# Kernel optimization log

Measured on AMD Instinct MI355X. Metric: run time of the kernel, lower is better.

Reference implementation:

```python
import jax, jax.numpy as jnp
import numpy as np

B, T, N, C, D = 8, 12, 1024, 64, 10

def setup_inputs() -> dict:
    key = jax.random.key(0)
    ks = jax.random.split(key, 7)
    x = jax.random.normal(ks[0], (B, T, N, C), dtype=jnp.float32)
    e1 = jax.random.normal(ks[1], (N, D), dtype=jnp.float32)
    e2 = jax.random.normal(ks[2], (N, D), dtype=jnp.float32)
    # buffer: sym-normalized adjacency after the __init__-time softmax
    A_sym = jax.random.uniform(ks[3], (N, N), dtype=jnp.float32)
    weights_pool = jax.random.normal(ks[4], (N, C, C), dtype=jnp.float32) * 0.02
    bias_pool = jax.random.normal(ks[5], (N, C), dtype=jnp.float32) * 0.02
    alpha = jnp.array([0.9], dtype=jnp.float32)
    beta = jnp.array([0.9], dtype=jnp.float32)
    gamma = jnp.array([0.1], dtype=jnp.float32)
    return {"x": x, "node_embeddings1": e1, "node_embeddings2": e2,
            "A_sym": A_sym, "weights_pool": weights_pool, "bias_pool": bias_pool,
            "alpha": alpha, "beta": beta, "gamma": gamma}


def reference(x, node_embeddings1, node_embeddings2, A_sym, weights_pool,
              bias_pool, alpha, beta, gamma):
    n = node_embeddings1.shape[0]
    # dynamic supports: relu(tanh(E1 E2^T - E2 E1^T)) + I
    s = jnp.tanh(node_embeddings1 @ node_embeddings2.T
                 - node_embeddings2 @ node_embeddings1.T)
    supports = jnp.eye(n, dtype=x.dtype) + jax.nn.relu(s)          # (N,N)

    # static branch: row-softmax of the precomputed sym-norm adjacency
    A = jax.nn.softmax(A_sym, axis=-1)                              # (N,N)
    x_static = jax.nn.relu(jnp.einsum('nm,btmc->btnc', A, x))       # (B,T,N,C)

    # spatial attention branch (note: softmax over the TIME axis, as in source)
    score = jnp.einsum('btnc,btmc->btnm', x, x)                     # (B,T,N,N)
    score = jax.nn.softmax(score, axis=1)
    x_sa = jax.nn.relu(jnp.einsum('btnm,btmc->btnc', score, x))     # (B,T,N,C)

    # adaptive graph conv: per-node weights/bias from supports
    weights = jnp.einsum('nd,dio->nio', supports, weights_pool)     # (N,C,C)
    bias = supports @ bias_pool                                     # (N,C)
    x_g = jnp.einsum('nm,btmc->btnc', supports, x)                  # (B,T,N,C)
    x_gconv = jax.nn.relu(jnp.einsum('btni,nio->btno', x_g, weights) + bias)

    return alpha * x_gconv + beta * x_sa + gamma * x_static
```

## Files before the change

### kernel.cpp

```cpp
#include <hip/hip_runtime.h>
#include <math.h>

#define Bdim 8
#define Tdim 12
#define BT   96
#define Ndim 1024
#define Cdim 64
#define Ddim 10
#define Jdim 6144
#define IOdim 4096

typedef __attribute__((ext_vector_type(4))) float f32x4;
typedef __attribute__((ext_vector_type(8))) short bf16x8;
typedef __attribute__((ext_vector_type(4))) _Float16 f16x4;

__device__ inline short f2bf(float f) {
    union { float f; unsigned u; } v; v.f = f;
    return (short)((v.u + 0x8000u) >> 16);
}
__device__ inline float bf2f(short s) {
    union { float f; unsigned u; } v; v.u = ((unsigned)(unsigned short)s) << 16;
    return v.f;
}
__device__ inline void load_lds16(const void* g, void* l) {
    __builtin_amdgcn_global_load_lds(
        (const __attribute__((address_space(1))) unsigned int*)g,
        (__attribute__((address_space(3))) unsigned int*)l, 16, 0, 0);
}
__device__ inline float fexp(float x) { return __expf(x); }
__device__ inline float frcp(float x) { return __builtin_amdgcn_rcpf(x); }
__device__ inline float flog(float x) { return __logf(x); }

__global__ __launch_bounds__(256) void k_supports(
    const float* __restrict__ e1, const float* __restrict__ e2,
    short* __restrict__ Sbf)
{
    int idx = blockIdx.x * 256 + threadIdx.x;
    int i = idx >> 10, j = idx & 1023;
    float s = 0.f;
#pragma unroll
    for (int d = 0; d < Ddim; ++d)
        s += e1[i * Ddim + d] * e2[j * Ddim + d]
           - e2[i * Ddim + d] * e1[j * Ddim + d];
    float t = 1.f - 2.f * frcp(fexp(2.f * s) + 1.f);
    float v = fmaxf(t, 0.f);
    if (i == j) v += 1.f;
    Sbf[idx] = f2bf(v);
}

__global__ __launch_bounds__(256) void k_softmax_rows(
    const float* __restrict__ In, short* __restrict__ Out)
{
    int row = blockIdx.x;
    const float* r = In + (size_t)row * Ndim;
    short* o = Out + (size_t)row * Ndim;
    __shared__ float red[256];
    int tid = threadIdx.x;
    float vals[4];
    float lmax = -INFINITY;
#pragma unroll
    for (int i = 0; i < 4; ++i) { vals[i] = r[tid + 256 * i]; lmax = fmaxf(lmax, vals[i]); }
    red[tid] = lmax; __syncthreads();
    for (int s = 128; s > 0; s >>= 1) {
        if (tid < s) red[tid] = fmaxf(red[tid], red[tid + s]);
        __syncthreads();
    }
    float m = red[0]; __syncthreads();
    float lsum = 0.f;
#pragma unroll
    for (int i = 0; i < 4; ++i) { vals[i] = fexp(vals[i] - m); lsum += vals[i]; }
    red[tid] = lsum; __syncthreads();
    for (int s = 128; s > 0; s >>= 1) {
        if (tid < s) red[tid] += red[tid + s];
        __syncthreads();
    }
    float inv = frcp(red[0]);
#pragma unroll
    for (int i = 0; i < 4; ++i) o[tid + 256 * i] = f2bf(vals[i] * inv);
}

__global__ __launch_bounds__(256) void k_cvt_x(
    const float* __restrict__ x, short* __restrict__ xbf, short* __restrict__ xT)
{
    __shared__ float Lt[64][65];
    int bt = blockIdx.y, n0 = blockIdx.x * 64;
    const float* src = x + (size_t)bt * 65536 + (size_t)n0 * 64;
    int tid = threadIdx.x;
#pragma unroll
    for (int p = 0; p < 4; ++p) {
        int idx = p * 256 + tid;
        int r = idx >> 4, c4 = idx & 15;
        float4 v = *(const float4*)&src[r * 64 + c4 * 4];
        short4 s4 = make_short4(f2bf(v.x), f2bf(v.y), f2bf(v.z), f2bf(v.w));
        *(short4*)&xbf[(size_t)bt * 65536 + (size_t)(n0 + r) * 64 + c4 * 4] = s4;
        Lt[r][c4 * 4 + 0] = v.x; Lt[r][c4 * 4 + 1] = v.y;
        Lt[r][c4 * 4 + 2] = v.z; Lt[r][c4 * 4 + 3] = v.w;
    }
    __syncthreads();
#pragma unroll
    for (int p = 0; p < 4; ++p) {
        int idx = p * 256 + tid;
        int c = idx >> 4, k4 = idx & 15;
        short4 s4 = make_short4(f2bf(Lt[k4 * 4 + 0][c]), f2bf(Lt[k4 * 4 + 1][c]),
                                f2bf(Lt[k4 * 4 + 2][c]), f2bf(Lt[k4 * 4 + 3][c]));
        *(short4*)&xT[(size_t)bt * 65536 + (size_t)c * 1024 + n0 + k4 * 4] = s4;
    }
}

__global__ __launch_bounds__(256) void k_cvt_wp(
    const float* __restrict__ wp, short* __restrict__ wpT)
{
    __shared__ float Lt[64][65];
    int k0 = blockIdx.y * 64, j0 = blockIdx.x * 64;
    int tid = threadIdx.x;
#pragma unroll
    for (int p = 0; p < 4; ++p) {
        int idx = p * 256 + tid;
        int r = idx >> 4, c4 = idx & 15;
        float4 v = *(const float4*)&wp[(size_t)(k0 + r) * IOdim + j0 + c4 * 4];
        Lt[r][c4 * 4 + 0] = v.x; Lt[r][c4 * 4 + 1] = v.y;
        Lt[r][c4 * 4 + 2] = v.z; Lt[r][c4 * 4 + 3] = v.w;
    }
    __syncthreads();
#pragma unroll
    for (int p = 0; p < 4; ++p) {
        int idx = p * 256 + tid;
        int c = idx >> 4, k4 = idx & 15;
        short4 s4 = make_short4(f2bf(Lt[k4 * 4 + 0][c]), f2bf(Lt[k4 * 4 + 1][c]),
                                f2bf(Lt[k4 * 4 + 2][c]), f2bf(Lt[k4 * 4 + 3][c]));
        *(short4*)&wpT[(size_t)(j0 + c) * 1024 + k0 + k4 * 4] = s4;
    }
}

__global__ __launch_bounds__(256) void k_cvt_bp(
    const float* __restrict__ bp, short* __restrict__ bpT)
{
    __shared__ float Lt[64][65];
    int k0 = blockIdx.x * 64;
    int tid = threadIdx.x;
#pragma unroll
    for (int p = 0; p < 4; ++p) {
        int idx = p * 256 + tid;
        int r = idx >> 4, c4 = idx & 15;
        float4 v = *(const float4*)&bp[(size_t)(k0 + r) * 64 + c4 * 4];
        Lt[r][c4 * 4 + 0] = v.x; Lt[r][c4 * 4 + 1] = v.y;
        Lt[r][c4 * 4 + 2] = v.z; Lt[r][c4 * 4 + 3] = v.w;
    }
    __syncthreads();
#pragma unroll
    for (int p = 0; p < 4; ++p) {
        int idx = p * 256 + tid;
        int c = idx >> 4, k4 = idx & 15;
        short4 s4 = make_short4(f2bf(Lt[k4 * 4 + 0][c]), f2bf(Lt[k4 * 4 + 1][c]),
                                f2bf(Lt[k4 * 4 + 2][c]), f2bf(Lt[k4 * 4 + 3][c]));
        *(short4*)&bpT[(size_t)c * 1024 + k0 + k4 * 4] = s4;
    }
}

template<int MODE>
__global__ __launch_bounds__(256) void k_gemm_bt(
    const short* __restrict__ A, const short* __restrict__ Bm,
    float* __restrict__ Cf, short* __restrict__ Cb,
    const float* __restrict__ gamma_p)
{
    __shared__ short At[128 * 64];
    __shared__ short Bt[128 * 64];
    const int tid = threadIdx.x;
    const int w = tid >> 6, l = tid & 63;
    const int l15 = l & 15, q = l >> 4;
    const int n0 = blockIdx.x * 128, j0 = blockIdx.y * 128;
    const int wr = (w & 1) * 64, wc = (w >> 1) * 64;
    const int lrow = l >> 3, lc8 = l & 7;

    f32x4 acc[4][4];
#pragma unroll
    for (int i = 0; i < 4; ++i)
#pragma unroll
        for (int j = 0; j < 4; ++j) acc[i][j] = (f32x4)0.f;

    for (int k0 = 0; k0 < 1024; k0 += 64) {
        __syncthreads();
#pragma unroll
        for (int p = 0; p < 4; ++p) {
            int r = p * 32 + w * 8 + lrow;
            int sc = lc8 ^ (r & 7);
            load_lds16(A + (size_t)(n0 + r) * 1024 + k0 + sc * 8,
                       &At[(p * 32 + w * 8) * 64]);
            load_lds16(Bm + (size_t)(j0 + r) * 1024 + k0 + sc * 8,
                       &Bt[(p * 32 + w * 8) * 64]);
        }
        __syncthreads();
#pragma unroll
        for (int ks = 0; ks < 2; ++ks) {
            bf16x8 af[4], bf[4];
#pragma unroll
            for (int rt = 0; rt < 4; ++rt) {
                int row = wr + rt * 16 + l15;
                int pos = (ks * 4 + q) ^ (row & 7);
                af[rt] = *(const bf16x8*)&At[row * 64 + pos * 8];
            }
#pragma unroll
            for (int ct = 0; ct < 4; ++ct) {
                int row = wc + ct * 16 + l15;
                int pos = (ks * 4 + q) ^ (row & 7);
                bf[ct] = *(const bf16x8*)&Bt[row * 64 + pos * 8];
            }
#pragma unroll
            for (int rt = 0; rt < 4; ++rt)
#pragma unroll
                for (int ct = 0; ct < 4; ++ct)
                    acc[rt][ct] = __builtin_amdgcn_mfma_f32_16x16x32_bf16(
                        af[rt], bf[ct], acc[rt][ct], 0, 0, 0);
        }
    }

    float gmm = (MODE == 0) ? gamma_p[0] : 0.f;
#pragma unroll
    for (int rt = 0; rt < 4; ++rt) {
        int nr = n0 + wr + rt * 16 + q * 4;
#pragma unroll
        for (int ct = 0; ct < 4; ++ct) {
            int j = j0 + wc + ct * 16 + l15;
#pragma unroll
            for (int r = 0; r < 4; ++r) {
                float v = acc[rt][ct][r];
                int n = nr + r;
                if (MODE == 1) {
                    Cb[(size_t)n * IOdim + j] = f2bf(v);
                } else if (n < 1024) {
                    int bt = j >> 6, c = j & 63;
                    Cf[(size_t)bt * 65536 + (size_t)n * 64 + c] = gmm * fmaxf(v, 0.f);
                } else {
                    Cb[(size_t)(n - 1024) * Jdim + j] = f2bf(v);
                }
            }
        }
    }
}

__global__ __launch_bounds__(256, 4) void k_sa_z(
    const short* __restrict__ xbf, short* __restrict__ Lh)
{
    __shared__ short Xn[64 * 64];
    __shared__ short Xm[64 * 64];

    int id = blockIdx.x;
    int b = id & 7;
    int r = id >> 3;
    int tn = r & 15, tm = r >> 4;
    int tid = threadIdx.x;
    int w = tid >> 6, l = tid & 63;
    int l15 = l & 15, q = l >> 4;
    int lrow = l >> 3, lc8 = l & 7;
    int n0 = tn * 64, m0 = tm * 64;
    int wn = (w & 1) * 32, wm = (w >> 1) * 32;

    const short* Xb = xbf + (size_t)b * Tdim * Ndim * Cdim;
    short* Lb = Lh + ((size_t)b << 20);

    f32x4 M[2][2], Z[2][2];
#pragma unroll
    for (int nh = 0; nh < 2; ++nh)
#pragma unroll
        for (int mh = 0; mh < 2; ++mh) { M[nh][mh] = (f32x4)(-INFINITY); Z[nh][mh] = (f32x4)0.f; }

    for (int t = 0; t < Tdim; ++t) {
        const short* xt = Xb + (size_t)t * (Ndim * Cdim);
        __syncthreads();
#pragma unroll
        for (int p = 0; p < 2; ++p) {
            int rr = p * 32 + w * 8 + lrow;
            int sc = lc8 ^ (rr & 7);
            load_lds16(xt + (size_t)(n0 + rr) * 64 + sc * 8, &Xn[(p * 32 + w * 8) * 64]);
            load_lds16(xt + (size_t)(m0 + rr) * 64 + sc * 8, &Xm[(p * 32 + w * 8) * 64]);
        }
        __syncthreads();

        f32x4 sacc[2][2];
        sacc[0][0] = (f32x4)0.f; sacc[0][1] = (f32x4)0.f;
        sacc[1][0] = (f32x4)0.f; sacc[1][1] = (f32x4)0.f;
#pragma unroll
        for (int ch = 0; ch < 2; ++ch) {
            bf16x8 qb[2], af[2];
#pragma unroll
            for (int nh = 0; nh < 2; ++nh) {
                int row = wn + nh * 16 + l15;
                int pos = (ch * 4 + q) ^ (row & 7);
                qb[nh] = *(const bf16x8*)&Xn[row * 64 + pos * 8];
            }
#pragma unroll
            for (int mh = 0; mh < 2; ++mh) {
                int row = wm + mh * 16 + l15;
                int pos = (ch * 4 + q) ^ (row & 7);
                af[mh] = *(const bf16x8*)&Xm[row * 64 + pos * 8];
            }
#pragma unroll
            for (int nh = 0; nh < 2; ++nh)
#pragma unroll
                for (int mh = 0; mh < 2; ++mh)
                    sacc[nh][mh] = __builtin_amdgcn_mfma_f32_16x16x32_bf16(
                        af[mh], qb[nh], sacc[nh][mh], 0, 0, 0);
        }
#pragma unroll
        for (int nh = 0; nh < 2; ++nh)
#pragma unroll
            for (int mh = 0; mh < 2; ++mh)
#pragma unroll
                for (int i = 0; i < 4; ++i) {
                    float s  = sacc[nh][mh][i];
                    float mo = M[nh][mh][i];
                    float mn = fmaxf(mo, s);
                    Z[nh][mh][i] = Z[nh][mh][i] * fexp(mo - mn) + fexp(s - mn);
                    M[nh][mh][i] = mn;
                }
    }
#pragma unroll
    for (int nh = 0; nh < 2; ++nh)
#pragma unroll
        for (int mh = 0; mh < 2; ++mh) {
            f16x4 ev;
#pragma unroll
            for (int i = 0; i < 4; ++i)
                ev[i] = (_Float16)(M[nh][mh][i] + flog(Z[nh][mh][i]));
            *(f16x4*)&Lb[(size_t)(n0 + wn + nh * 16 + l15) * 1024
                         + m0 + wm + mh * 16 + q * 4] = ev;
        }
}

__global__ __launch_bounds__(256, 3) void k_sa_pv(
    const short* __restrict__ xbf, const short* __restrict__ xT,
    const short* __restrict__ Lh, float* __restrict__ Out,
    const float* __restrict__ beta_p)
{
    __shared__ short Xm[2][64 * 72];
    __shared__ short XTl[2][64 * 72];
    __shared__ short Pl[4][16][72];

    int id = blockIdx.x;
    int b = id & 7;
    int r = id >> 3;
    int nt = r & 7, t = r >> 3;
    int tid = threadIdx.x;
    int w = tid >> 6, l = tid & 63;
    int l15 = l & 15, q = l >> 4;
    int n0 = nt * 128 + w * 32;

    const short* Xb  = xbf + ((size_t)b * Tdim + t) * (Ndim * Cdim);
    const short* XTb = xT  + ((size_t)b * Tdim + t) * (Ndim * Cdim);
    const short* Lb  = Lh + ((size_t)b << 20);

    int srow = tid >> 2, sc4 = tid & 3;

    bf16x8 qf[2][2];
#pragma unroll
    for (int nh = 0; nh < 2; ++nh)
#pragma unroll
        for (int ch = 0; ch < 2; ++ch)
            qf[nh][ch] = *(const bf16x8*)&Xb[(n0 + nh * 16 + l15) * 64 + ch * 32 + q * 8];

    f32x4 oacc[2][4];
#pragma unroll
    for (int nh = 0; nh < 2; ++nh)
#pragma unroll
        for (int ct = 0; ct < 4; ++ct) oacc[nh][ct] = (f32x4)0.f;

    bf16x8 v[2], v2[2];
#pragma unroll
    for (int p = 0; p < 2; ++p) {
        v[p]  = *(const bf16x8*)&Xb[(size_t)srow * 64 + (sc4 + 4 * p) * 8];
        v2[p] = *(const bf16x8*)&XTb[(size_t)srow * 1024 + (sc4 + 4 * p) * 8];
    }

    for (int mi = 0; mi < 16; ++mi) {
        int cur = mi & 1;
        int m0 = mi * 64;
#pragma unroll
        for (int p = 0; p < 2; ++p) {
            *(bf16x8*)&Xm[cur][srow * 72 + (sc4 + 4 * p) * 8]  = v[p];
            *(bf16x8*)&XTl[cur][srow * 72 + (sc4 + 4 * p) * 8] = v2[p];
        }
        int m0n = (mi < 15) ? m0 + 64 : m0;
#pragma unroll
        for (int p = 0; p < 2; ++p) {
            v[p]  = *(const bf16x8*)&Xb[(size_t)(m0n + srow) * 64 + (sc4 + 4 * p) * 8];
            v2[p] = *(const bf16x8*)&XTb[(size_t)srow * 1024 + m0n + (sc4 + 4 * p) * 8];
        }
        f16x4 e[2][4];
#pragma unroll
        for (int nh = 0; nh < 2; ++nh)
#pragma unroll
            for (int mh = 0; mh < 4; ++mh)
                e[nh][mh] = *(const f16x4*)&Lb[(size_t)(n0 + nh * 16 + l15) * 1024
                                               + m0 + mh * 16 + q * 4];
        __syncthreads();

        f32x4 sacc[2][4];
#pragma unroll
        for (int nh = 0; nh < 2; ++nh)
#pragma unroll
            for (int mh = 0; mh < 4; ++mh) sacc[nh][mh] = (f32x4)0.f;
#pragma unroll
        for (int ch = 0; ch < 2; ++ch) {
#pragma unroll
            for (int mh = 0; mh < 4; ++mh) {
                bf16x8 af = *(const bf16x8*)&Xm[cur][(mh * 16 + l15) * 72 + ch * 32 + q * 8];
                sacc[0][mh] = __builtin_amdgcn_mfma_f32_16x16x32_bf16(
                    af, qf[0][ch], sacc[0][mh], 0, 0, 0);
                sacc[1][mh] = __builtin_amdgcn_mfma_f32_16x16x32_bf16(
                    af, qf[1][ch], sacc[1][mh], 0, 0, 0);
            }
        }
#pragma unroll
        for (int nh = 0; nh < 2; ++nh) {
#pragma unroll
            for (int mh = 0; mh < 4; ++mh) {
                f32x4 p = sacc[nh][mh];
                f16x4 ee = e[nh][mh];
                unsigned u0 = (unsigned)(unsigned short)f2bf(fexp(p[0] - (float)ee[0]))
                            | ((unsigned)(unsigned short)f2bf(fexp(p[1] - (float)ee[1])) << 16);
                unsigned u1 = (unsigned)(unsigned short)f2bf(fexp(p[2] - (float)ee[2]))
                            | ((unsigned)(unsigned short)f2bf(fexp(p[3] - (float)ee[3])) << 16);
                *(uint2*)&Pl[w][l15][mh * 16 + q * 4] = make_uint2(u0, u1);
            }
#pragma unroll
            for (int ks = 0; ks < 2; ++ks) {
                bf16x8 pf = *(const bf16x8*)&Pl[w][l15][ks * 32 + q * 8];
#pragma unroll
                for (int ct = 0; ct < 4; ++ct) {
                    bf16x8 bfr = *(const bf16x8*)&XTl[cur][(ct * 16 + l15) * 72 + ks * 32 + q * 8];
                    oacc[nh][ct] = __builtin_amdgcn_mfma_f32_16x16x32_bf16(
                        pf, bfr, oacc[nh][ct], 0, 0, 0);
                }
            }
        }
    }

    float beta = beta_p[0];
#pragma unroll
    for (int nh = 0; nh < 2; ++nh)
#pragma unroll
        for (int ct = 0; ct < 4; ++ct)
#pragma unroll
            for (int r2 = 0; r2 < 4; ++r2) {
                size_t idx = (((size_t)b * Tdim + t) * Ndim + n0 + nh * 16 + q * 4 + r2) * Cdim
                           + ct * 16 + l15;
                Out[idx] += beta * fmaxf(oacc[nh][ct][r2], 0.f);
            }
}

__global__ __launch_bounds__(256) void k_bias(
    const short* __restrict__ Sbf, const short* __restrict__ bpT,
    float* __restrict__ bias)
{
    int tid = threadIdx.x;
    int w = tid >> 6, l = tid & 63;
    int l15 = l & 15, q = l >> 4;
    int nr = blockIdx.x * 64 + w * 16;

    f32x4 acc[4];
#pragma unroll
    for (int ct = 0; ct < 4; ++ct) acc[ct] = (f32x4)0.f;

    for (int k0 = 0; k0 < 1024; k0 += 32) {
        bf16x8 af = *(const bf16x8*)&Sbf[(size_t)(nr + l15) * 1024 + k0 + q * 8];
#pragma unroll
        for (int ct = 0; ct < 4; ++ct) {
            bf16x8 bf = *(const bf16x8*)&bpT[(size_t)(ct * 16 + l15) * 1024 + k0 + q * 8];
            acc[ct] = __builtin_amdgcn_mfma_f32_16x16x32_bf16(af, bf, acc[ct], 0, 0, 0);
        }
    }
#pragma unroll
    for (int ct = 0; ct < 4; ++ct)
#pragma unroll
        for (int r = 0; r < 4; ++r)
            bias[(size_t)(nr + q * 4 + r) * 64 + ct * 16 + l15] = acc[ct][r];
}

__global__ __launch_bounds__(384) void k_gconv(
    const short* __restrict__ xgT, const short* __restrict__ Wb,
    const float* __restrict__ bias, float* __restrict__ Out,
    const float* __restrict__ alpha_p)
{
    __shared__ short Wl[64 * 64];
    int n = blockIdx.x;
    int tid = threadIdx.x;
    for (int f = tid; f < 512; f += 384) {
        int k = f >> 3, j = f & 7;
        *(bf16x8*)&Wl[k * 64 + (j ^ ((k >> 3) & 7)) * 8] =
            *(const bf16x8*)&Wb[(size_t)n * IOdim + f * 8];
    }
    __syncthreads();
    int w = tid / 64, l = tid & 63, l15 = l & 15, q = l >> 4;
    f32x4 acc[4];
#pragma unroll
    for (int ct = 0; ct < 4; ++ct) acc[ct] = (f32x4)0.f;
    const short* xr = xgT + (size_t)n * Jdim + (size_t)(w * 16 + l15) * 64;
#pragma unroll
    for (int ks = 0; ks < 2; ++ks) {
        bf16x8 a = *(const bf16x8*)&xr[ks * 32 + q * 8];
        int kb = ks * 32 + q * 8;
        int msk = (kb >> 3) & 7;
#pragma unroll
        for (int ct = 0; ct < 4; ++ct) {
            bf16x8 bfr;
#pragma unroll
            for (int e = 0; e < 8; ++e) {
                int o = ct * 16 + l15;
                bfr[e] = Wl[(kb + e) * 64 + (((o >> 3) ^ msk) * 8) + (o & 7)];
            }
            acc[ct] = __builtin_amdgcn_mfma_f32_16x16x32_bf16(a, bfr, acc[ct], 0, 0, 0);
        }
    }
    float alpha = alpha_p[0];
#pragma unroll
    for (int ct = 0; ct < 4; ++ct) {
        int o = ct * 16 + l15;
        float bo = bias[(size_t)n * 64 + o];
#pragma unroll
        for (int r = 0; r < 4; ++r) {
            int bt = w * 16 + q * 4 + r;
            size_t idx = (size_t)bt * 65536 + (size_t)n * 64 + o;
            Out[idx] += alpha * fmaxf(acc[ct][r] + bo, 0.f);
        }
    }
}

extern "C" void kernel_launch(void* const* d_in, const int* in_sizes, int n_in,
                              void* d_out, int out_size, void* d_ws, size_t ws_size,
                              hipStream_t stream)
{
    const float* x     = (const float*)d_in[0];
    const float* e1    = (const float*)d_in[1];
    const float* e2    = (const float*)d_in[2];
    const float* Asym  = (const float*)d_in[3];
    const float* wpool = (const float*)d_in[4];
    const float* bpool = (const float*)d_in[5];
    const float* alpha = (const float*)d_in[6];
    const float* beta  = (const float*)d_in[7];
    const float* gamma = (const float*)d_in[8];
    float* out = (float*)d_out;

    short* ASbf = (short*)d_ws;
    short* xbf  = ASbf + 2048 * 1024;
    short* xT   = xbf  + 6291456;
    short* wpT  = xT   + 6291456;
    short* Wbf  = wpT  + 4194304;
    short* xgT  = Wbf  + 4194304;
    float* bias = (float*)(xgT + 6291456);
    short* Lh   = (short*)(bias + 65536);
    short* bpT  = Lh + 8388608;

    k_supports<<<4096, 256, 0, stream>>>(e1, e2, ASbf + 1024 * 1024);
    k_softmax_rows<<<1024, 256, 0, stream>>>(Asym, ASbf);
    k_cvt_x<<<dim3(16, 96), 256, 0, stream>>>(x, xbf, xT);
    k_cvt_wp<<<dim3(64, 16), 256, 0, stream>>>(wpool, wpT);
    k_cvt_bp<<<16, 256, 0, stream>>>(bpool, bpT);
    k_sa_z<<<2048, 256, 0, stream>>>(xbf, Lh);
    k_gemm_bt<0><<<dim3(16, 48), 256, 0, stream>>>(ASbf, xT, out, xgT, gamma);
    k_gemm_bt<1><<<dim3(8, 32), 256, 0, stream>>>(ASbf + 1024 * 1024, wpT, nullptr, Wbf, nullptr);
    k_bias<<<16, 256, 0, stream>>>(ASbf + 1024 * 1024, bpT, bias);
    k_sa_pv<<<768, 256, 0, stream>>>(xbf, xT, Lh, out, beta);
    k_gconv<<<1024, 384, 0, stream>>>(xgT, Wbf, bias, out, alpha);
}
```

Baseline: 322.3 us.

## Exploit score symmetry in logsumexp kernel and swizzle LDS in PV kernel

The time-axis logsumexp of x x^T is symmetric in (n,m), so k_sa_z now computes only upper-triangular 64x64 tiles (1088 blocks instead of 2048) and writes each result both to its own position and to the transposed position. This roughly halves the score GEMMs and exp work in that kernel, at the cost of scattered 2-byte transposed stores. Separately, k_sa_pv replaces padded LDS rows (stride 72) with an XOR-swizzled stride-64 layout for Xm, XTl and the P staging buffer. That targets bank conflicts and reduces LDS footprint.

```diff
diff --git a/kernel.cpp b/kernel.cpp
--- a/kernel.cpp
+++ b/kernel.cpp
@@ -247,7 +247,9 @@
     int id = blockIdx.x;
     int b = id & 7;
     int r = id >> 3;
-    int tn = r & 15, tm = r >> 4;
+    int tn = 0, rr = r;
+    while (rr >= 16 - tn) { rr -= 16 - tn; ++tn; }
+    int tm = tn + rr;
     int tid = threadIdx.x;
     int w = tid >> 6, l = tid & 63;
     int l15 = l & 15, q = l >> 4;
@@ -269,10 +271,10 @@
         __syncthreads();
 #pragma unroll
         for (int p = 0; p < 2; ++p) {
-            int rr = p * 32 + w * 8 + lrow;
-            int sc = lc8 ^ (rr & 7);
-            load_lds16(xt + (size_t)(n0 + rr) * 64 + sc * 8, &Xn[(p * 32 + w * 8) * 64]);
-            load_lds16(xt + (size_t)(m0 + rr) * 64 + sc * 8, &Xm[(p * 32 + w * 8) * 64]);
+            int rw = p * 32 + w * 8 + lrow;
+            int sc = lc8 ^ (rw & 7);
+            load_lds16(xt + (size_t)(n0 + rw) * 64 + sc * 8, &Xn[(p * 32 + w * 8) * 64]);
+            load_lds16(xt + (size_t)(m0 + rw) * 64 + sc * 8, &Xm[(p * 32 + w * 8) * 64]);
         }
         __syncthreads();
 
@@ -322,8 +324,14 @@
 #pragma unroll
             for (int i = 0; i < 4; ++i)
                 ev[i] = (_Float16)(M[nh][mh][i] + flog(Z[nh][mh][i]));
-            *(f16x4*)&Lb[(size_t)(n0 + wn + nh * 16 + l15) * 1024
-                         + m0 + wm + mh * 16 + q * 4] = ev;
+            int nn = n0 + wn + nh * 16 + l15;
+            int mm = m0 + wm + mh * 16 + q * 4;
+            *(f16x4*)&Lb[(size_t)nn * 1024 + mm] = ev;
+            if (tn != tm) {
+#pragma unroll
+                for (int i = 0; i < 4; ++i)
+                    Lb[(size_t)(mm + i) * 1024 + nn] = ((short*)&ev)[i];
+            }
         }
 }
 
@@ -332,9 +340,9 @@
     const short* __restrict__ Lh, float* __restrict__ Out,
     const float* __restrict__ beta_p)
 {
-    __shared__ short Xm[2][64 * 72];
-    __shared__ short XTl[2][64 * 72];
-    __shared__ short Pl[4][16][72];
+    __shared__ short Xm[2][64 * 64];
+    __shared__ short XTl[2][64 * 64];
+    __shared__ short Pl[4][16 * 64];
 
     int id = blockIdx.x;
     int b = id & 7;
@@ -376,8 +384,10 @@
         int m0 = mi * 64;
 #pragma unroll
         for (int p = 0; p < 2; ++p) {
-            *(bf16x8*)&Xm[cur][srow * 72 + (sc4 + 4 * p) * 8]  = v[p];
-            *(bf16x8*)&XTl[cur][srow * 72 + (sc4 + 4 * p) * 8] = v2[p];
+            int g = sc4 + 4 * p;
+            int pos = g ^ (srow & 7);
+            *(bf16x8*)&Xm[cur][srow * 64 + pos * 8]  = v[p];
+            *(bf16x8*)&XTl[cur][srow * 64 + pos * 8] = v2[p];
         }
         int m0n = (mi < 15) ? m0 + 64 : m0;
 #pragma unroll
@@ -403,7 +413,9 @@
         for (int ch = 0; ch < 2; ++ch) {
 #pragma unroll
             for (int mh = 0; mh < 4; ++mh) {
-                bf16x8 af = *(const bf16x8*)&Xm[cur][(mh * 16 + l15) * 72 + ch * 32 + q * 8];
+                int row = mh * 16 + l15;
+                int pos = (ch * 4 + q) ^ (row & 7);
+                bf16x8 af = *(const bf16x8*)&Xm[cur][row * 64 + pos * 8];
                 sacc[0][mh] = __builtin_amdgcn_mfma_f32_16x16x32_bf16(
                     af, qf[0][ch], sacc[0][mh], 0, 0, 0);
                 sacc[1][mh] = __builtin_amdgcn_mfma_f32_16x16x32_bf16(
@@ -420,14 +432,20 @@
                             | ((unsigned)(unsigned short)f2bf(fexp(p[1] - (float)ee[1])) << 16);
                 unsigned u1 = (unsigned)(unsigned short)f2bf(fexp(p[2] - (float)ee[2]))
                             | ((unsigned)(unsigned short)f2bf(fexp(p[3] - (float)ee[3])) << 16);
-                *(uint2*)&Pl[w][l15][mh * 16 + q * 4] = make_uint2(u0, u1);
+                int g = mh * 2 + (q >> 1);
+                int pos = g ^ (l15 & 7);
+                *(uint2*)&Pl[w][l15 * 64 + pos * 8 + (q & 1) * 4] = make_uint2(u0, u1);
             }
 #pragma unroll
             for (int ks = 0; ks < 2; ++ks) {
-                bf16x8 pf = *(const bf16x8*)&Pl[w][l15][ks * 32 + q * 8];
+                int gr = ks * 4 + q;
+                int pos = gr ^ (l15 & 7);
+                bf16x8 pf = *(const bf16x8*)&Pl[w][l15 * 64 + pos * 8];
 #pragma unroll
                 for (int ct = 0; ct < 4; ++ct) {
-                    bf16x8 bfr = *(const bf16x8*)&XTl[cur][(ct * 16 + l15) * 72 + ks * 32 + q * 8];
+                    int row = ct * 16 + l15;
+                    int bp = (ks * 4 + q) ^ (row & 7);
+                    bf16x8 bfr = *(const bf16x8*)&XTl[cur][row * 64 + bp * 8];
                     oacc[nh][ct] = __builtin_amdgcn_mfma_f32_16x16x32_bf16(
                         pf, bfr, oacc[nh][ct], 0, 0, 0);
                 }
@@ -555,7 +573,7 @@
     k_cvt_x<<<dim3(16, 96), 256, 0, stream>>>(x, xbf, xT);
     k_cvt_wp<<<dim3(64, 16), 256, 0, stream>>>(wpool, wpT);
     k_cvt_bp<<<16, 256, 0, stream>>>(bpool, bpT);
-    k_sa_z<<<2048, 256, 0, stream>>>(xbf, Lh);
+    k_sa_z<<<1088, 256, 0, stream>>>(xbf, Lh);
     k_gemm_bt<0><<<dim3(16, 48), 256, 0, stream>>>(ASbf, xT, out, xgT, gamma);
     k_gemm_bt<1><<<dim3(8, 32), 256, 0, stream>>>(ASbf + 1024 * 1024, wpT, nullptr, Wbf, nullptr);
     k_bias<<<16, 256, 0, stream>>>(ASbf + 1024 * 1024, bpT, bias);
```

After: 311.9 us. -3.2%, faster.
